# Kernel tuning notes

Measured on AMD Instinct MI355X. Metric: run time of the kernel, lower is better.

Reference implementation:

```python
import jax, jax.numpy as jnp
import numpy as np

C = 1.0
MIN_NORM = 1e-15
BALL_EPS = 4e-3  # hgcn eps for float32 in proj

def _norm(v):
    return jnp.maximum(jnp.linalg.norm(v, axis=-1, keepdims=True), MIN_NORM)

def artanh(y):
    return jnp.arctanh(jnp.clip(y, -1.0 + 1e-7, 1.0 - 1e-7))

def logmap0(p, c):
    sqrt_c = c ** 0.5
    pn = _norm(p)
    return p / (sqrt_c * pn) * artanh(sqrt_c * pn)

def expmap0(u, c):
    sqrt_c = c ** 0.5
    un = _norm(u)
    return jnp.tanh(sqrt_c * un) * u / (sqrt_c * un)

def proj(x, c):
    xn = _norm(x)
    maxnorm = (1.0 - BALL_EPS) / (c ** 0.5)
    return jnp.where(xn > maxnorm, x / xn * maxnorm, x)

def setup_inputs() -> dict:
    key = jax.random.key(0)
    k1, k2, k3, k4 = jax.random.split(key, 4)
    N, E, F = 100000, 640000, 128
    # points inside the Poincare ball
    x = 0.01 * jax.random.normal(k1, (N, F), dtype=jnp.float32)
    adj = jax.random.randint(k2, (2, E), 0, N, dtype=jnp.int64)
    edge_attr = jax.random.normal(k3, (E, F), dtype=jnp.float32)
    att_w = jax.random.normal(k4, (1, 3 * F), dtype=jnp.float32) * (1.0 / np.sqrt(3 * F))
    att_b = jnp.zeros((1,), dtype=jnp.float32)
    return {"x": x, "adj": adj, "edge_attr": edge_attr, "att_w": att_w, "att_b": att_b}

def reference(x, adj, edge_attr, att_w, att_b):
    N = x.shape[0]
    src, dst = adj[0], adj[1]  # agg_direction='in' -> i = 0
    xt = logmap0(x, C)  # [N, F] tangent features
    xs = xt[src]        # [E, F] gathered neighbor tangent feats
    # DenseAtt: sigmoid(Linear(cat(x_i, x_j, edge_attr)))
    feats = jnp.concatenate([xs, xt[dst], edge_attr], axis=-1)  # [E, 3F]
    adj_att = jax.nn.sigmoid(feats @ att_w.T + att_b)           # [E, 1]
    ones = jnp.ones((src.shape[0], 1), dtype=xt.dtype)
    agg_add = jax.ops.segment_sum(xs * adj_att, src, num_segments=N)
    cnt_src = jnp.maximum(jax.ops.segment_sum(ones, src, num_segments=N), 1.0)
    cnt_dst = jnp.maximum(jax.ops.segment_sum(ones, dst, num_segments=N), 1.0)
    mean_src = jax.ops.segment_sum(edge_attr, src, num_segments=N) / cnt_src
    mean_dst = jax.ops.segment_sum(edge_attr, dst, num_segments=N) / cnt_dst
    support_t = xt + agg_add + mean_src + mean_dst
    return proj(expmap0(support_t, C), C)
```

## Files before the change

kernel.cpp:

```cpp
#include <hip/hip_runtime.h>
#include <math.h>

#define F 128
#define WAVE 64
#define CAP 64
#define LSLOT 32

__global__ void k_zero(int* __restrict__ p, int n) {
    int i = blockIdx.x * blockDim.x + threadIdx.x;
    if (i < n) p[i] = 0;
}

__device__ __forceinline__ float halfwave_reduce_sum(float v) {
#pragma unroll
    for (int off = 16; off >= 1; off >>= 1)
        v += __shfl_xor(v, off, 64);
    return v;
}

__global__ void k_prenode(const float* __restrict__ x, const float* __restrict__ w,
                          float* __restrict__ a_s, float* __restrict__ a_d, int N) {
    int row = blockIdx.x * (blockDim.x >> 5) + (threadIdx.x >> 5);
    int fl = threadIdx.x & 31;
    if (row >= N) return;
    float4 v = ((const float4*)(x + (size_t)row * F))[fl];
    float ss = halfwave_reduce_sum(v.x * v.x + v.y * v.y + v.z * v.z + v.w * v.w);
    float pn = fmaxf(sqrtf(ss), 1e-15f);
    float y = fminf(pn, 1.0f - 1e-7f);
    float at = 0.5f * logf((1.0f + y) / (1.0f - y));
    float s = at / pn;
    float4 o = make_float4(v.x * s, v.y * s, v.z * s, v.w * s);
    float4 W0 = ((const float4*)w)[fl];
    float4 W1 = ((const float4*)(w + F))[fl];
    float d0 = halfwave_reduce_sum(o.x * W0.x + o.y * W0.y + o.z * W0.z + o.w * W0.w);
    float d1 = halfwave_reduce_sum(o.x * W1.x + o.y * W1.y + o.z * W1.z + o.w * W1.w);
    if (fl == 0) { a_s[row] = d0; a_d[row] = d1; }
}

__global__ void k_fill(const int* __restrict__ src, const int* __restrict__ dst,
                       int* __restrict__ cur_src, int* __restrict__ cur_dst,
                       int* __restrict__ elist_src, int* __restrict__ elist_dst, int E) {
    int e = blockIdx.x * blockDim.x + threadIdx.x;
    if (e >= E) return;
    int s = src[e], d = dst[e];
    int ps = atomicAdd(&cur_src[s], 1);
    if (ps < CAP) elist_src[(size_t)s * CAP + ps] = e;
    int pd = atomicAdd(&cur_dst[d], 1);
    if (pd < CAP) elist_dst[(size_t)d * CAP + pd] = e;
}

__global__ __launch_bounds__(128) void
k_aggfinal(const float* __restrict__ x, const float* __restrict__ eattr,
           const int* __restrict__ dst,
           const int* __restrict__ cur_src, const int* __restrict__ cur_dst,
           const int* __restrict__ elist_src, const int* __restrict__ elist_dst,
           const float* __restrict__ a_s, const float* __restrict__ a_d,
           const float* __restrict__ w, const float* __restrict__ bptr,
           float* __restrict__ out, int N) {
    __shared__ float dot_lds[2][LSLOT * 33];
    int wid  = threadIdx.x >> 6;
    int lane = threadIdx.x & (WAVE - 1);
    int n = blockIdx.x * 2 + wid;
    if (n >= N) return;
    float* dlds = dot_lds[wid];
    int half = lane >> 5;
    int fl   = lane & 31;

    int cS = cur_src[n]; int degS = cS < CAP ? cS : CAP;
    int cD = cur_dst[n]; int degD = cD < CAP ? cD : CAP;
    int e_lnS = (lane < degS) ? elist_src[(size_t)n * CAP + lane] : 0;
    int e_lnD = (lane < degD) ? elist_dst[(size_t)n * CAP + lane] : 0;
    int dstv  = (lane < degS) ? dst[e_lnS] : 0;
    float advl = (lane < degS) ? a_d[dstv] : 0.f;

    float4 W2 = ((const float4*)(w + 2 * F))[fl];
    float a_sn = a_s[n];
    float bias = bptr[0];

    float4 accS = make_float4(0.f, 0.f, 0.f, 0.f);
    float4 accD = make_float4(0.f, 0.f, 0.f, 0.f);
    float attsum_fb = 0.f;
    int degM = degS > degD ? degS : degD;
    for (int i = 0; i < degM; i += 2) {
        int idx = i + half;
        int eS = __shfl(e_lnS, idx, 64);
        int eD = __shfl(e_lnD, idx, 64);
        float adv = __shfl(advl, idx, 64);
        if (idx < degD) {
            float4 v = ((const float4*)(eattr + (size_t)eD * F))[fl];
            accD.x += v.x; accD.y += v.y; accD.z += v.z; accD.w += v.w;
        }
        if (idx < degS) {
            float4 v = ((const float4*)(eattr + (size_t)eS * F))[fl];
            accS.x += v.x; accS.y += v.y; accS.z += v.z; accS.w += v.w;
            float p = v.x * W2.x + v.y * W2.y + v.z * W2.z + v.w * W2.w;
            if (idx < LSLOT) {
                dlds[idx * 33 + fl] = p;
            } else {
                float dotv = halfwave_reduce_sum(p);
                attsum_fb += 1.0f / (1.0f + __expf(-(a_sn + adv + dotv + bias)));
            }
        }
    }
    accS.x += __shfl_xor(accS.x, 32, 64); accS.y += __shfl_xor(accS.y, 32, 64);
    accS.z += __shfl_xor(accS.z, 32, 64); accS.w += __shfl_xor(accS.w, 32, 64);
    accD.x += __shfl_xor(accD.x, 32, 64); accD.y += __shfl_xor(accD.y, 32, 64);
    accD.z += __shfl_xor(accD.z, 32, 64); accD.w += __shfl_xor(accD.w, 32, 64);
    attsum_fb += __shfl_xor(attsum_fb, 32, 64);

    int mS = degS < LSLOT ? degS : LSLOT;
    float att_l = 0.f;
    if (lane < mS) {
        float dotv = 0.f;
#pragma unroll
        for (int k = 0; k < 32; ++k)
            dotv += dlds[lane * 33 + k];
        att_l = 1.0f / (1.0f + __expf(-(a_sn + advl + dotv + bias)));
    }
    float attsum = att_l;
#pragma unroll
    for (int off = 32; off >= 1; off >>= 1)
        attsum += __shfl_xor(attsum, off, 64);
    attsum += attsum_fb;

    float4 xv = ((const float4*)(x + (size_t)n * F))[fl];
    float ssx = halfwave_reduce_sum(xv.x * xv.x + xv.y * xv.y + xv.z * xv.z + xv.w * xv.w);
    float pnx = fmaxf(sqrtf(ssx), 1e-15f);
    float yx = fminf(pnx, 1.0f - 1e-7f);
    float atx = 0.5f * logf((1.0f + yx) / (1.0f - yx));
    float sx = atx / pnx;

    float invS = 1.0f / fmaxf((float)cS, 1.0f);
    float invD = 1.0f / fmaxf((float)cD, 1.0f);
    float fa = (1.0f + attsum) * sx;
    float4 u;
    u.x = xv.x * fa + accS.x * invS + accD.x * invD;
    u.y = xv.y * fa + accS.y * invS + accD.y * invD;
    u.z = xv.z * fa + accS.z * invS + accD.z * invD;
    u.w = xv.w * fa + accS.w * invS + accD.w * invD;

    float pp = halfwave_reduce_sum(u.x * u.x + u.y * u.y + u.z * u.z + u.w * u.w);
    float un = fmaxf(sqrtf(pp), 1e-15f);
    float t = tanhf(un);
    float scale = fminf(t, 1.0f - 4e-3f) / un;
    if (half == 0) {
        float4 o = make_float4(u.x * scale, u.y * scale, u.z * scale, u.w * scale);
        ((float4*)(out + (size_t)n * F))[fl] = o;
    }
}

extern "C" void kernel_launch(void* const* d_in, const int* in_sizes, int n_in,
                              void* d_out, int out_size, void* d_ws, size_t ws_size,
                              hipStream_t stream) {
    const float* x      = (const float*)d_in[0];
    const int*   adj    = (const int*)d_in[1];
    const float* eattr  = (const float*)d_in[2];
    const float* att_w  = (const float*)d_in[3];
    const float* att_b  = (const float*)d_in[4];
    float* out = (float*)d_out;

    const int N = in_sizes[0] / F;
    const int E = in_sizes[1] / 2;
    const int* src = adj;
    const int* dst = adj + E;

    char* ws = (char*)d_ws;
    size_t off = 0;
    float* a_s       = (float*)(ws + off); off += (size_t)N * sizeof(float);
    float* a_d       = (float*)(ws + off); off += (size_t)N * sizeof(float);
    int*   elist_src = (int*)  (ws + off); off += (size_t)N * CAP * sizeof(int);
    int*   elist_dst = (int*)  (ws + off); off += (size_t)N * CAP * sizeof(int);
    int*   zblock    = (int*)  (ws + off);
    int*   cur_src   = zblock;
    int*   cur_dst   = zblock + N;

    dim3 blk(256);
    const int HPB = 256 / 32;

    k_zero    <<<(2 * N + 255) / 256, blk, 0, stream>>>(zblock, 2 * N);
    k_prenode <<<(N + HPB - 1) / HPB, blk, 0, stream>>>(x, att_w, a_s, a_d, N);
    k_fill    <<<(E + 255) / 256, blk, 0, stream>>>(src, dst, cur_src, cur_dst,
                                                    elist_src, elist_dst, E);
    k_aggfinal<<<(N + 1) / 2, dim3(128), 0, stream>>>(x, eattr, dst,
                cur_src, cur_dst, elist_src, elist_dst, a_s, a_d, att_w, att_b, out, N);
}
```

Before: 272.3 us.

## Precompute per-edge a_d, unroll edge gather loop, use fast log/tanh

The fill kernel now writes a per-edge copy of a_d[dst], so the aggregation kernel does one dependent load per edge instead of two chained loads (dst then a_d). The edge-attribute gather loop is unrolled by two with separate accumulators to keep more loads in flight. The LDS dot-product sum is split into four partial sums. Accurate logf and tanhf are replaced with __logf and an exp-based tanh. The cost is an extra E-sized workspace write, a small change in float rounding, and higher register pressure.

```diff
diff --git a/kernel.cpp b/kernel.cpp
--- a/kernel.cpp
+++ b/kernel.cpp
@@ -27,7 +27,7 @@
     float ss = halfwave_reduce_sum(v.x * v.x + v.y * v.y + v.z * v.z + v.w * v.w);
     float pn = fmaxf(sqrtf(ss), 1e-15f);
     float y = fminf(pn, 1.0f - 1e-7f);
-    float at = 0.5f * logf((1.0f + y) / (1.0f - y));
+    float at = 0.5f * __logf((1.0f + y) / (1.0f - y));
     float s = at / pn;
     float4 o = make_float4(v.x * s, v.y * s, v.z * s, v.w * s);
     float4 W0 = ((const float4*)w)[fl];
@@ -38,11 +38,14 @@
 }
 
 __global__ void k_fill(const int* __restrict__ src, const int* __restrict__ dst,
+                       const float* __restrict__ a_d,
                        int* __restrict__ cur_src, int* __restrict__ cur_dst,
-                       int* __restrict__ elist_src, int* __restrict__ elist_dst, int E) {
+                       int* __restrict__ elist_src, int* __restrict__ elist_dst,
+                       float* __restrict__ ad_e, int E) {
     int e = blockIdx.x * blockDim.x + threadIdx.x;
     if (e >= E) return;
     int s = src[e], d = dst[e];
+    ad_e[e] = a_d[d];
     int ps = atomicAdd(&cur_src[s], 1);
     if (ps < CAP) elist_src[(size_t)s * CAP + ps] = e;
     int pd = atomicAdd(&cur_dst[d], 1);
@@ -51,10 +54,9 @@
 
 __global__ __launch_bounds__(128) void
 k_aggfinal(const float* __restrict__ x, const float* __restrict__ eattr,
-           const int* __restrict__ dst,
            const int* __restrict__ cur_src, const int* __restrict__ cur_dst,
            const int* __restrict__ elist_src, const int* __restrict__ elist_dst,
-           const float* __restrict__ a_s, const float* __restrict__ a_d,
+           const float* __restrict__ a_s, const float* __restrict__ ad_e,
            const float* __restrict__ w, const float* __restrict__ bptr,
            float* __restrict__ out, int N) {
     __shared__ float dot_lds[2][LSLOT * 33];
@@ -70,38 +72,60 @@
     int cD = cur_dst[n]; int degD = cD < CAP ? cD : CAP;
     int e_lnS = (lane < degS) ? elist_src[(size_t)n * CAP + lane] : 0;
     int e_lnD = (lane < degD) ? elist_dst[(size_t)n * CAP + lane] : 0;
-    int dstv  = (lane < degS) ? dst[e_lnS] : 0;
-    float advl = (lane < degS) ? a_d[dstv] : 0.f;
+    float advl = (lane < degS) ? ad_e[e_lnS] : 0.f;
 
     float4 W2 = ((const float4*)(w + 2 * F))[fl];
     float a_sn = a_s[n];
     float bias = bptr[0];
 
-    float4 accS = make_float4(0.f, 0.f, 0.f, 0.f);
-    float4 accD = make_float4(0.f, 0.f, 0.f, 0.f);
+    float4 accS0 = make_float4(0.f, 0.f, 0.f, 0.f), accS1 = accS0;
+    float4 accD0 = accS0, accD1 = accS0;
     float attsum_fb = 0.f;
     int degM = degS > degD ? degS : degD;
-    for (int i = 0; i < degM; i += 2) {
-        int idx = i + half;
-        int eS = __shfl(e_lnS, idx, 64);
-        int eD = __shfl(e_lnD, idx, 64);
-        float adv = __shfl(advl, idx, 64);
-        if (idx < degD) {
-            float4 v = ((const float4*)(eattr + (size_t)eD * F))[fl];
-            accD.x += v.x; accD.y += v.y; accD.z += v.z; accD.w += v.w;
-        }
-        if (idx < degS) {
-            float4 v = ((const float4*)(eattr + (size_t)eS * F))[fl];
-            accS.x += v.x; accS.y += v.y; accS.z += v.z; accS.w += v.w;
+    for (int i = 0; i < degM; i += 4) {
+        int idx0 = i + half;
+        int idx1 = i + 2 + half;
+        int eS0 = __shfl(e_lnS, idx0, 64);
+        int eS1 = __shfl(e_lnS, idx1, 64);
+        int eD0 = __shfl(e_lnD, idx0, 64);
+        int eD1 = __shfl(e_lnD, idx1, 64);
+        if (idx0 < degD) {
+            float4 v = ((const float4*)(eattr + (size_t)eD0 * F))[fl];
+            accD0.x += v.x; accD0.y += v.y; accD0.z += v.z; accD0.w += v.w;
+        }
+        if (idx1 < degD) {
+            float4 v = ((const float4*)(eattr + (size_t)eD1 * F))[fl];
+            accD1.x += v.x; accD1.y += v.y; accD1.z += v.z; accD1.w += v.w;
+        }
+        if (idx0 < degS) {
+            float4 v = ((const float4*)(eattr + (size_t)eS0 * F))[fl];
+            accS0.x += v.x; accS0.y += v.y; accS0.z += v.z; accS0.w += v.w;
             float p = v.x * W2.x + v.y * W2.y + v.z * W2.z + v.w * W2.w;
-            if (idx < LSLOT) {
-                dlds[idx * 33 + fl] = p;
+            if (idx0 < LSLOT) {
+                dlds[idx0 * 33 + fl] = p;
             } else {
+                float adv = __shfl(advl, idx0, 64);
                 float dotv = halfwave_reduce_sum(p);
                 attsum_fb += 1.0f / (1.0f + __expf(-(a_sn + adv + dotv + bias)));
             }
         }
+        if (idx1 < degS) {
+            float4 v = ((const float4*)(eattr + (size_t)eS1 * F))[fl];
+            accS1.x += v.x; accS1.y += v.y; accS1.z += v.z; accS1.w += v.w;
+            float p = v.x * W2.x + v.y * W2.y + v.z * W2.z + v.w * W2.w;
+            if (idx1 < LSLOT) {
+                dlds[idx1 * 33 + fl] = p;
+            } else {
+                float adv = __shfl(advl, idx1, 64);
+                float dotv = halfwave_reduce_sum(p);
+                attsum_fb += 1.0f / (1.0f + __expf(-(a_sn + adv + dotv + bias)));
+            }
+        }
     }
+    float4 accS = make_float4(accS0.x + accS1.x, accS0.y + accS1.y,
+                              accS0.z + accS1.z, accS0.w + accS1.w);
+    float4 accD = make_float4(accD0.x + accD1.x, accD0.y + accD1.y,
+                              accD0.z + accD1.z, accD0.w + accD1.w);
     accS.x += __shfl_xor(accS.x, 32, 64); accS.y += __shfl_xor(accS.y, 32, 64);
     accS.z += __shfl_xor(accS.z, 32, 64); accS.w += __shfl_xor(accS.w, 32, 64);
     accD.x += __shfl_xor(accD.x, 32, 64); accD.y += __shfl_xor(accD.y, 32, 64);
@@ -111,10 +135,15 @@
     int mS = degS < LSLOT ? degS : LSLOT;
     float att_l = 0.f;
     if (lane < mS) {
-        float dotv = 0.f;
+        float d0 = 0.f, d1 = 0.f, d2 = 0.f, d3 = 0.f;
 #pragma unroll
-        for (int k = 0; k < 32; ++k)
-            dotv += dlds[lane * 33 + k];
+        for (int k = 0; k < 32; k += 4) {
+            d0 += dlds[lane * 33 + k];
+            d1 += dlds[lane * 33 + k + 1];
+            d2 += dlds[lane * 33 + k + 2];
+            d3 += dlds[lane * 33 + k + 3];
+        }
+        float dotv = (d0 + d1) + (d2 + d3);
         att_l = 1.0f / (1.0f + __expf(-(a_sn + advl + dotv + bias)));
     }
     float attsum = att_l;
@@ -127,7 +156,7 @@
     float ssx = halfwave_reduce_sum(xv.x * xv.x + xv.y * xv.y + xv.z * xv.z + xv.w * xv.w);
     float pnx = fmaxf(sqrtf(ssx), 1e-15f);
     float yx = fminf(pnx, 1.0f - 1e-7f);
-    float atx = 0.5f * logf((1.0f + yx) / (1.0f - yx));
+    float atx = 0.5f * __logf((1.0f + yx) / (1.0f - yx));
     float sx = atx / pnx;
 
     float invS = 1.0f / fmaxf((float)cS, 1.0f);
@@ -141,7 +170,8 @@
 
     float pp = halfwave_reduce_sum(u.x * u.x + u.y * u.y + u.z * u.z + u.w * u.w);
     float un = fmaxf(sqrtf(pp), 1e-15f);
-    float t = tanhf(un);
+    float ex = __expf(2.0f * un);
+    float t = 1.0f - 2.0f / (ex + 1.0f);
     float scale = fminf(t, 1.0f - 4e-3f) / un;
     if (half == 0) {
         float4 o = make_float4(u.x * scale, u.y * scale, u.z * scale, u.w * scale);
@@ -168,6 +198,7 @@
     size_t off = 0;
     float* a_s       = (float*)(ws + off); off += (size_t)N * sizeof(float);
     float* a_d       = (float*)(ws + off); off += (size_t)N * sizeof(float);
+    float* ad_e      = (float*)(ws + off); off += (size_t)E * sizeof(float);
     int*   elist_src = (int*)  (ws + off); off += (size_t)N * CAP * sizeof(int);
     int*   elist_dst = (int*)  (ws + off); off += (size_t)N * CAP * sizeof(int);
     int*   zblock    = (int*)  (ws + off);
@@ -179,8 +210,8 @@
 
     k_zero    <<<(2 * N + 255) / 256, blk, 0, stream>>>(zblock, 2 * N);
     k_prenode <<<(N + HPB - 1) / HPB, blk, 0, stream>>>(x, att_w, a_s, a_d, N);
-    k_fill    <<<(E + 255) / 256, blk, 0, stream>>>(src, dst, cur_src, cur_dst,
-                                                    elist_src, elist_dst, E);
-    k_aggfinal<<<(N + 1) / 2, dim3(128), 0, stream>>>(x, eattr, dst,
-                cur_src, cur_dst, elist_src, elist_dst, a_s, a_d, att_w, att_b, out, N);
-}
+    k_fill    <<<(E + 255) / 256, blk, 0, stream>>>(src, dst, a_d, cur_src, cur_dst,
+                                                    elist_src, elist_dst, ad_e, E);
+    k_aggfinal<<<(N + 1) / 2, dim3(128), 0, stream>>>(x, eattr,
+                cur_src, cur_dst, elist_src, elist_dst, a_s, ad_e, att_w, att_b, out, N);
+}
```

Measured after the change: 259.9 us. -4.5%, faster.
